# Kernel optimization log

Measured on AMD Instinct MI355X. Metric: run time of the kernel, lower is better.

## Reference

```python
import jax, jax.numpy as jnp
import numpy as np

INPUT_DIM = 768
HIDDEN = 64
NUM_CLASSES = 1


def _uniform(key, shape, bound):
    return jax.random.uniform(key, shape, jnp.float32, -bound, bound)


def setup_inputs() -> dict:
    key = jax.random.key(0)
    ks = jax.random.split(key, 16)
    B, T = 128, 512
    bound = 1.0 / np.sqrt(HIDDEN)  # PyTorch RNN init range
    inp = {
        "x": jax.random.normal(ks[0], (B, T, INPUT_DIM), jnp.float32),
        "fixation_num": 1,
        # layer 0: input_dim -> hidden
        "W_ih0": _uniform(ks[1], (HIDDEN, INPUT_DIM), bound),
        "W_hh0": _uniform(ks[2], (HIDDEN, HIDDEN), bound),
        "b_ih0": _uniform(ks[3], (HIDDEN,), bound),
        "b_hh0": _uniform(ks[4], (HIDDEN,), bound),
        # layer 1
        "W_ih1": _uniform(ks[5], (HIDDEN, HIDDEN), bound),
        "W_hh1": _uniform(ks[6], (HIDDEN, HIDDEN), bound),
        "b_ih1": _uniform(ks[7], (HIDDEN,), bound),
        "b_hh1": _uniform(ks[8], (HIDDEN,), bound),
        # layer 2
        "W_ih2": _uniform(ks[9], (HIDDEN, HIDDEN), bound),
        "W_hh2": _uniform(ks[10], (HIDDEN, HIDDEN), bound),
        "b_ih2": _uniform(ks[11], (HIDDEN,), bound),
        "b_hh2": _uniform(ks[12], (HIDDEN,), bound),
        # final linear head
        "fc_w": _uniform(ks[13], (NUM_CLASSES, HIDDEN), bound),
        "fc_b": _uniform(ks[14], (NUM_CLASSES,), bound),
    }
    return inp


def _rnn_layer(x, W_ih, W_hh, b_ih, b_hh):
    # x: [B, T, In] -> hidden sequence [B, T, H]; vanilla tanh RNN, h0 = 0
    pre = jnp.einsum("bti,hi->bth", x, W_ih) + b_ih + b_hh  # input projection for all t
    B = x.shape[0]
    h0 = jnp.zeros((B, W_hh.shape[0]), x.dtype)

    def step(h, p_t):  # p_t: [B, H]
        h = jnp.tanh(p_t + h @ W_hh.T)
        return h, h

    _, hs = jax.lax.scan(step, h0, jnp.swapaxes(pre, 0, 1))  # hs: [T, B, H]
    return jnp.swapaxes(hs, 0, 1)


def reference(x, fixation_num, W_ih0, W_hh0, b_ih0, b_hh0,
              W_ih1, W_hh1, b_ih1, b_hh1,
              W_ih2, W_hh2, b_ih2, b_hh2, fc_w, fc_b):
    # fixation_num is unused by the original forward
    h = _rnn_layer(x, W_ih0, W_hh0, b_ih0, b_hh0)
    h = _rnn_layer(h, W_ih1, W_hh1, b_ih1, b_hh1)
    h = _rnn_layer(h, W_ih2, W_hh2, b_ih2, b_hh2)
    last = h[:, -1, :]  # [B, H]
    return last @ fc_w.T + fc_b  # [B, num_classes]
```

## Files before the change

### kernel.cpp

```cpp
#include <hip/hip_runtime.h>


typedef __fp16 h2_t __attribute__((ext_vector_type(2)));
typedef __fp16 h8_t __attribute__((ext_vector_type(8)));
typedef float  f4_t __attribute__((ext_vector_type(4)));

union F4H  { float4 f; h2_t h[4]; };
union F4H8 { float4 f; h8_t h8; h2_t h2[4]; };
union H8U  { h2_t h2[4]; h8_t h8; };

__device__ __forceinline__ float fdot2(h2_t a, h2_t b, float c) {
    return __builtin_amdgcn_fdot2(a, b, c, false);
}
__device__ __forceinline__ h2_t pack_h2(float x, float y) {
    return __builtin_amdgcn_cvt_pkrtz(x, y);
}
__device__ __forceinline__ float tanh_fast(float x) {
    float e = __expf(2.0f * x);
    return 1.0f - 2.0f * __builtin_amdgcn_rcpf(e + 1.0f);
}

__global__ __launch_bounds__(256) void gemm_pre0(
    const float* __restrict__ x,
    const float* __restrict__ Wih,
    const float* __restrict__ bih, const float* __restrict__ bhh,
    float* __restrict__ pre0)
{
    const int tid = threadIdx.x;
    const int wv  = tid >> 6;
    const int l   = tid & 63;
    const int m   = l & 15;
    const int q   = l >> 4;
    const int rowB = blockIdx.x * 128 + wv * 32;

    const float* ax0 = x + (size_t)(rowB + m) * 768 + q * 8;
    const float* ax1 = x + (size_t)(rowB + 16 + m) * 768 + q * 8;

    float4 ar[2][2];
    float4 br[4][2];

    ar[0][0] = *(const float4*)ax0;       ar[0][1] = *(const float4*)(ax0 + 4);
    ar[1][0] = *(const float4*)ax1;       ar[1][1] = *(const float4*)(ax1 + 4);
#pragma unroll
    for (int nt = 0; nt < 4; ++nt) {
        const float* p = Wih + (size_t)(nt * 16 + m) * 768 + q * 8;
        br[nt][0] = *(const float4*)p;    br[nt][1] = *(const float4*)(p + 4);
    }

    f4_t acc[2][4];
#pragma unroll
    for (int mt = 0; mt < 2; ++mt)
#pragma unroll
        for (int nt = 0; nt < 4; ++nt)
#pragma unroll
            for (int i = 0; i < 4; ++i) acc[mt][nt][i] = 0.0f;

#pragma unroll
    for (int it = 0; it < 24; ++it) {
        H8U fa[2], fb[4];
#pragma unroll
        for (int mt = 0; mt < 2; ++mt) {
            fa[mt].h2[0] = pack_h2(ar[mt][0].x, ar[mt][0].y);
            fa[mt].h2[1] = pack_h2(ar[mt][0].z, ar[mt][0].w);
            fa[mt].h2[2] = pack_h2(ar[mt][1].x, ar[mt][1].y);
            fa[mt].h2[3] = pack_h2(ar[mt][1].z, ar[mt][1].w);
        }
#pragma unroll
        for (int nt = 0; nt < 4; ++nt) {
            fb[nt].h2[0] = pack_h2(br[nt][0].x, br[nt][0].y);
            fb[nt].h2[1] = pack_h2(br[nt][0].z, br[nt][0].w);
            fb[nt].h2[2] = pack_h2(br[nt][1].x, br[nt][1].y);
            fb[nt].h2[3] = pack_h2(br[nt][1].z, br[nt][1].w);
        }
        if (it + 1 < 24) {
            const int ko = (it + 1) * 32;
            ar[0][0] = *(const float4*)(ax0 + ko);
            ar[0][1] = *(const float4*)(ax0 + ko + 4);
            ar[1][0] = *(const float4*)(ax1 + ko);
            ar[1][1] = *(const float4*)(ax1 + ko + 4);
#pragma unroll
            for (int nt = 0; nt < 4; ++nt) {
                const float* p = Wih + (size_t)(nt * 16 + m) * 768 + q * 8 + ko;
                br[nt][0] = *(const float4*)p;
                br[nt][1] = *(const float4*)(p + 4);
            }
        }
#pragma unroll
        for (int mt = 0; mt < 2; ++mt)
#pragma unroll
            for (int nt = 0; nt < 4; ++nt)
                acc[mt][nt] = __builtin_amdgcn_mfma_f32_16x16x32_f16(
                    fa[mt].h8, fb[nt].h8, acc[mt][nt], 0, 0, 0);
    }

    float bn[4];
#pragma unroll
    for (int nt = 0; nt < 4; ++nt) bn[nt] = bih[nt * 16 + m] + bhh[nt * 16 + m];
#pragma unroll
    for (int mt = 0; mt < 2; ++mt)
#pragma unroll
        for (int i = 0; i < 4; ++i) {
            int row = rowB + mt * 16 + q * 4 + i;
            float* pr = pre0 + (size_t)row * 64 + m;
#pragma unroll
            for (int nt = 0; nt < 4; ++nt)
                pr[nt * 16] = acc[mt][nt][i] + bn[nt];
        }
}

__device__ __forceinline__ float layer_epoch(
    const __fp16* __restrict__ in0,
    __fp16* __restrict__ self0, int par,
    const h2_t* wB2, const h8_t* wX, float* __restrict__ xb,
    float bias, int j)
{
    __fp16*       selfPar  = self0 + par * 512;
    const __fp16* selfPrev = self0 + (par ^ 1) * 512;
    const int mm = j & 15;
    const int q4 = j >> 4;

    F4H8 A0, A1;
    const __fp16* arow = in0 + mm * 64 + q4 * 8;
    A0.f = *(const float4*)arow;
    A1.f = *(const float4*)(arow + 32);

    f4_t xacc[4];
#pragma unroll
    for (int nt = 0; nt < 4; ++nt) {
#pragma unroll
        for (int i = 0; i < 4; ++i) xacc[nt][i] = 0.0f;
        xacc[nt] = __builtin_amdgcn_mfma_f32_16x16x32_f16(
            A0.h8, wX[nt * 2 + 0], xacc[nt], 0, 0, 0);
        xacc[nt] = __builtin_amdgcn_mfma_f32_16x16x32_f16(
            A1.h8, wX[nt * 2 + 1], xacc[nt], 0, 0, 0);
    }
    if (j < 32) {
#pragma unroll
        for (int nt = 0; nt < 4; ++nt)
#pragma unroll
            for (int i = 0; i < 4; ++i)
                xb[(q4 * 4 + i) * 64 + nt * 16 + mm] = xacc[nt][i];
    }

    float hN = 0.0f;
#pragma unroll
    for (int s = 0; s < 8; ++s) {
        const __fp16* rc = (s == 0) ? (selfPrev + 7 * 64) : (selfPar + (s - 1) * 64);
        F4H uh[8];
#pragma unroll
        for (int qq = 0; qq < 8; ++qq) uh[qq].f = *(const float4*)(rc + qq * 8);
        float xs = xb[s * 64 + j];

        float a0 = 0.f, a1 = 0.f, a2 = 0.f, a3 = 0.f;
#pragma unroll
        for (int qq = 0; qq < 8; ++qq) {
            a0 = fdot2(wB2[qq * 4 + 0], uh[qq].h[0], a0);
            a1 = fdot2(wB2[qq * 4 + 1], uh[qq].h[1], a1);
            a2 = fdot2(wB2[qq * 4 + 2], uh[qq].h[2], a2);
            a3 = fdot2(wB2[qq * 4 + 3], uh[qq].h[3], a3);
        }
        hN = tanh_fast((a0 + a1) + (a2 + a3) + xs + bias);
        selfPar[s * 64 + j] = (__fp16)hN;
    }
    return hN;
}

__global__ __launch_bounds__(192, 1) void rnn_fused(
    const float* __restrict__ pre0,
    const float* __restrict__ Whh0,
    const float* __restrict__ Wih1, const float* __restrict__ Whh1,
    const float* __restrict__ bih1, const float* __restrict__ bhh1,
    const float* __restrict__ Wih2, const float* __restrict__ Whh2,
    const float* __restrict__ bih2, const float* __restrict__ bhh2,
    const float* __restrict__ fcw, const float* __restrict__ fcb,
    float* __restrict__ out)
{
    const int tid = threadIdx.x;
    const int g   = tid >> 6;
    const int j   = tid & 63;
    const int b   = blockIdx.x;

    __shared__ __align__(16) __fp16 hb[3][2][8][64];
    __shared__ __align__(16) float  xb2[2][8][64];

    const float* WB = (g == 0) ? Whh0 : ((g == 1) ? Whh1 : Whh2);
    h2_t wB2[32];
#pragma unroll
    for (int i = 0; i < 32; ++i)
        wB2[i] = pack_h2(WB[j * 64 + 2 * i], WB[j * 64 + 2 * i + 1]);

    const float* WX = (g == 1) ? Wih1 : ((g == 2) ? Wih2 : Whh0);
    const int mm = j & 15, q4 = j >> 4;
    h8_t wX[8];
#pragma unroll
    for (int nt = 0; nt < 4; ++nt)
#pragma unroll
        for (int c = 0; c < 2; ++c) {
            const float* p = WX + (nt * 16 + mm) * 64 + c * 32 + q4 * 8;
            float4 r0 = *(const float4*)p;
            float4 r1 = *(const float4*)(p + 4);
            H8U u;
            u.h2[0] = pack_h2(r0.x, r0.y); u.h2[1] = pack_h2(r0.z, r0.w);
            u.h2[2] = pack_h2(r1.x, r1.y); u.h2[3] = pack_h2(r1.z, r1.w);
            wX[nt * 2 + c] = u.h8;
        }

    const float bias = (g == 0) ? 0.0f
                     : ((g == 1) ? (bih1[j] + bhh1[j]) : (bih2[j] + bhh2[j]));

#pragma unroll
    for (int i = 0; i < 8; ++i) ((unsigned int*)hb)[tid + 192 * i] = 0u;

    const size_t pbase = (size_t)b * 32768;
    float pc[8], pn[8];
    if (g == 0) {
#pragma unroll
        for (int s = 0; s < 8; ++s) pc[s] = pre0[pbase + s * 64 + j];
    }
    __syncthreads();

    float hLast = 0.0f;

    for (int e = 0; e < 66; ++e) {
        if (g == 0) {
            if (e < 64) {
                if (e < 63) {
#pragma unroll
                    for (int s = 0; s < 8; ++s)
                        pn[s] = pre0[pbase + (size_t)(e + 1) * 512 + s * 64 + j];
                }
                const int par = e & 1;
#pragma unroll
                for (int s = 0; s < 8; ++s) {
                    const __fp16* rc = (s == 0) ? hb[0][par ^ 1][7] : hb[0][par][s - 1];
                    float a0 = 0.f, a1 = 0.f, a2 = 0.f, a3 = 0.f;
#pragma unroll
                    for (int qq = 0; qq < 8; ++qq) {
                        F4H u; u.f = *(const float4*)&rc[qq * 8];
                        a0 = fdot2(wB2[qq * 4 + 0], u.h[0], a0);
                        a1 = fdot2(wB2[qq * 4 + 1], u.h[1], a1);
                        a2 = fdot2(wB2[qq * 4 + 2], u.h[2], a2);
                        a3 = fdot2(wB2[qq * 4 + 3], u.h[3], a3);
                    }
                    float hN = tanh_fast((a0 + a1) + (a2 + a3) + pc[s]);
                    hb[0][par][s][j] = (__fp16)hN;
                }
#pragma unroll
                for (int s = 0; s < 8; ++s) pc[s] = pn[s];
            }
        } else if (g == 1) {
            if (e >= 1 && e < 65) {
                const int par = (e - 1) & 1;
                layer_epoch(&hb[0][par][0][0], &hb[1][0][0][0], par,
                            wB2, wX, &xb2[0][0][0], bias, j);
            }
        } else {
            if (e >= 2) {
                const int par = e & 1;
                float hN = layer_epoch(&hb[1][par][0][0], &hb[2][0][0][0], par,
                                       wB2, wX, &xb2[1][0][0], bias, j);
                if (e == 65) hLast = hN;
            }
        }
        __syncthreads();
    }

    if (g == 2) {
        float v = hLast * fcw[j];
#pragma unroll
        for (int m = 1; m < 64; m <<= 1) v += __shfl_xor(v, m, 64);
        if (j == 0) out[b] = v + fcb[0];
    }
}

extern "C" void kernel_launch(void* const* d_in, const int* in_sizes, int n_in,
                              void* d_out, int out_size, void* d_ws, size_t ws_size,
                              hipStream_t stream) {
    const float* x    = (const float*)d_in[0];
    const float* Wih0 = (const float*)d_in[2];
    const float* Whh0 = (const float*)d_in[3];
    const float* bih0 = (const float*)d_in[4];
    const float* bhh0 = (const float*)d_in[5];
    const float* Wih1 = (const float*)d_in[6];
    const float* Whh1 = (const float*)d_in[7];
    const float* bih1 = (const float*)d_in[8];
    const float* bhh1 = (const float*)d_in[9];
    const float* Wih2 = (const float*)d_in[10];
    const float* Whh2 = (const float*)d_in[11];
    const float* bih2 = (const float*)d_in[12];
    const float* bhh2 = (const float*)d_in[13];
    const float* fcw  = (const float*)d_in[14];
    const float* fcb  = (const float*)d_in[15];
    float* out  = (float*)d_out;
    float* pre0 = (float*)d_ws;

    gemm_pre0<<<512, 256, 0, stream>>>(x, Wih0, bih0, bhh0, pre0);
    rnn_fused<<<128, 192, 0, stream>>>(pre0, Whh0, Wih1, Whh1, bih1, bhh1,
                                       Wih2, Whh2, bih2, bhh2, fcw, fcb, out);
}
```

Before: 430.5 us.

## Prepack W_ih0 to fp16 fragments, shrink GEMM tile, widen RNN epochs to 16 steps

Adds a small kernel that converts W_ih0 once into fp16 MFMA fragments in workspace, so the input-projection GEMM loads packed B fragments instead of converting fp32 weights in every block. The GEMM uses 16 rows per wave with a two-deep register prefetch, doubling the grid. The fused 3-layer RNN pipeline now runs 16 timesteps per epoch instead of 8, halving the number of epochs and block-wide barriers, and the layer bias is folded into the MFMA projection output. Costs are more registers and LDS per block, plus an extra kernel launch.

```diff
diff --git a/kernel.cpp b/kernel.cpp
--- a/kernel.cpp
+++ b/kernel.cpp
@@ -20,9 +20,26 @@
     return 1.0f - 2.0f * __builtin_amdgcn_rcpf(e + 1.0f);
 }
 
+__global__ __launch_bounds__(256) void pack_wih(
+    const float* __restrict__ W, h8_t* __restrict__ wp)
+{
+    const int id = blockIdx.x * 256 + threadIdx.x;
+    if (id >= 24 * 4 * 64) return;
+    const int l  = id & 63;
+    const int nt = (id >> 6) & 3;
+    const int c  = id >> 8;
+    const float* p = W + (size_t)(nt * 16 + (l & 15)) * 768 + c * 32 + (l >> 4) * 8;
+    float4 r0 = *(const float4*)p;
+    float4 r1 = *(const float4*)(p + 4);
+    H8U u;
+    u.h2[0] = pack_h2(r0.x, r0.y); u.h2[1] = pack_h2(r0.z, r0.w);
+    u.h2[2] = pack_h2(r1.x, r1.y); u.h2[3] = pack_h2(r1.z, r1.w);
+    wp[id] = u.h8;
+}
+
 __global__ __launch_bounds__(256) void gemm_pre0(
     const float* __restrict__ x,
-    const float* __restrict__ Wih,
+    const h8_t* __restrict__ wp,
     const float* __restrict__ bih, const float* __restrict__ bhh,
     float* __restrict__ pre0)
 {
@@ -31,91 +48,74 @@
     const int l   = tid & 63;
     const int m   = l & 15;
     const int q   = l >> 4;
-    const int rowB = blockIdx.x * 128 + wv * 32;
-
-    const float* ax0 = x + (size_t)(rowB + m) * 768 + q * 8;
-    const float* ax1 = x + (size_t)(rowB + 16 + m) * 768 + q * 8;
+    const int rowB = blockIdx.x * 64 + wv * 16;
+
+    const float* ax = x + (size_t)(rowB + m) * 768 + q * 8;
 
     float4 ar[2][2];
-    float4 br[4][2];
-
-    ar[0][0] = *(const float4*)ax0;       ar[0][1] = *(const float4*)(ax0 + 4);
-    ar[1][0] = *(const float4*)ax1;       ar[1][1] = *(const float4*)(ax1 + 4);
-#pragma unroll
-    for (int nt = 0; nt < 4; ++nt) {
-        const float* p = Wih + (size_t)(nt * 16 + m) * 768 + q * 8;
-        br[nt][0] = *(const float4*)p;    br[nt][1] = *(const float4*)(p + 4);
-    }
-
-    f4_t acc[2][4];
-#pragma unroll
-    for (int mt = 0; mt < 2; ++mt)
+    h8_t   bf[2][4];
+
+#pragma unroll
+    for (int c = 0; c < 2; ++c) {
+        ar[c][0] = *(const float4*)(ax + c * 32);
+        ar[c][1] = *(const float4*)(ax + c * 32 + 4);
+        const int cb = c * 256 + l;
+        bf[c][0] = wp[cb];        bf[c][1] = wp[cb + 64];
+        bf[c][2] = wp[cb + 128];  bf[c][3] = wp[cb + 192];
+    }
+
+    f4_t acc[4];
+#pragma unroll
+    for (int nt = 0; nt < 4; ++nt)
+#pragma unroll
+        for (int i = 0; i < 4; ++i) acc[nt][i] = 0.0f;
+
+#pragma unroll
+    for (int it = 0; it < 24; ++it) {
+        const int bs = it & 1;
+        H8U fa;
+        fa.h2[0] = pack_h2(ar[bs][0].x, ar[bs][0].y);
+        fa.h2[1] = pack_h2(ar[bs][0].z, ar[bs][0].w);
+        fa.h2[2] = pack_h2(ar[bs][1].x, ar[bs][1].y);
+        fa.h2[3] = pack_h2(ar[bs][1].z, ar[bs][1].w);
+        h8_t fb0 = bf[bs][0], fb1 = bf[bs][1], fb2 = bf[bs][2], fb3 = bf[bs][3];
+
+        if (it + 2 < 24) {
+            const int ko = (it + 2) * 32;
+            ar[bs][0] = *(const float4*)(ax + ko);
+            ar[bs][1] = *(const float4*)(ax + ko + 4);
+            const int cb = (it + 2) * 256 + l;
+            bf[bs][0] = wp[cb];        bf[bs][1] = wp[cb + 64];
+            bf[bs][2] = wp[cb + 128];  bf[bs][3] = wp[cb + 192];
+        }
+
+        acc[0] = __builtin_amdgcn_mfma_f32_16x16x32_f16(fa.h8, fb0, acc[0], 0, 0, 0);
+        acc[1] = __builtin_amdgcn_mfma_f32_16x16x32_f16(fa.h8, fb1, acc[1], 0, 0, 0);
+        acc[2] = __builtin_amdgcn_mfma_f32_16x16x32_f16(fa.h8, fb2, acc[2], 0, 0, 0);
+        acc[3] = __builtin_amdgcn_mfma_f32_16x16x32_f16(fa.h8, fb3, acc[3], 0, 0, 0);
+    }
+
+    float bn[4];
+#pragma unroll
+    for (int nt = 0; nt < 4; ++nt) bn[nt] = bih[nt * 16 + m] + bhh[nt * 16 + m];
+#pragma unroll
+    for (int i = 0; i < 4; ++i) {
+        int row = rowB + q * 4 + i;
+        float* pr = pre0 + (size_t)row * 64 + m;
 #pragma unroll
         for (int nt = 0; nt < 4; ++nt)
-#pragma unroll
-            for (int i = 0; i < 4; ++i) acc[mt][nt][i] = 0.0f;
-
-#pragma unroll
-    for (int it = 0; it < 24; ++it) {
-        H8U fa[2], fb[4];
-#pragma unroll
-        for (int mt = 0; mt < 2; ++mt) {
-            fa[mt].h2[0] = pack_h2(ar[mt][0].x, ar[mt][0].y);
-            fa[mt].h2[1] = pack_h2(ar[mt][0].z, ar[mt][0].w);
-            fa[mt].h2[2] = pack_h2(ar[mt][1].x, ar[mt][1].y);
-            fa[mt].h2[3] = pack_h2(ar[mt][1].z, ar[mt][1].w);
-        }
-#pragma unroll
-        for (int nt = 0; nt < 4; ++nt) {
-            fb[nt].h2[0] = pack_h2(br[nt][0].x, br[nt][0].y);
-            fb[nt].h2[1] = pack_h2(br[nt][0].z, br[nt][0].w);
-            fb[nt].h2[2] = pack_h2(br[nt][1].x, br[nt][1].y);
-            fb[nt].h2[3] = pack_h2(br[nt][1].z, br[nt][1].w);
-        }
-        if (it + 1 < 24) {
-            const int ko = (it + 1) * 32;
-            ar[0][0] = *(const float4*)(ax0 + ko);
-            ar[0][1] = *(const float4*)(ax0 + ko + 4);
-            ar[1][0] = *(const float4*)(ax1 + ko);
-            ar[1][1] = *(const float4*)(ax1 + ko + 4);
-#pragma unroll
-            for (int nt = 0; nt < 4; ++nt) {
-                const float* p = Wih + (size_t)(nt * 16 + m) * 768 + q * 8 + ko;
-                br[nt][0] = *(const float4*)p;
-                br[nt][1] = *(const float4*)(p + 4);
-            }
-        }
-#pragma unroll
-        for (int mt = 0; mt < 2; ++mt)
-#pragma unroll
-            for (int nt = 0; nt < 4; ++nt)
-                acc[mt][nt] = __builtin_amdgcn_mfma_f32_16x16x32_f16(
-                    fa[mt].h8, fb[nt].h8, acc[mt][nt], 0, 0, 0);
-    }
-
-    float bn[4];
-#pragma unroll
-    for (int nt = 0; nt < 4; ++nt) bn[nt] = bih[nt * 16 + m] + bhh[nt * 16 + m];
-#pragma unroll
-    for (int mt = 0; mt < 2; ++mt)
-#pragma unroll
-        for (int i = 0; i < 4; ++i) {
-            int row = rowB + mt * 16 + q * 4 + i;
-            float* pr = pre0 + (size_t)row * 64 + m;
-#pragma unroll
-            for (int nt = 0; nt < 4; ++nt)
-                pr[nt * 16] = acc[mt][nt][i] + bn[nt];
-        }
+            pr[nt * 16] = acc[nt][i] + bn[nt];
+    }
 }
 
 __device__ __forceinline__ float layer_epoch(
     const __fp16* __restrict__ in0,
     __fp16* __restrict__ self0, int par,
     const h2_t* wB2, const h8_t* wX, float* __restrict__ xb,
-    float bias, int j)
+    const float* bias4, int j)
 {
-    __fp16*       selfPar  = self0 + par * 512;
-    const __fp16* selfPrev = self0 + (par ^ 1) * 512;
+    __fp16*       selfPar  = self0 + par * 1024;
+    const __fp16* selfPrev = self0 + (par ^ 1) * 1024;
     const int mm = j & 15;
     const int q4 = j >> 4;
 
@@ -134,22 +134,23 @@
         xacc[nt] = __builtin_amdgcn_mfma_f32_16x16x32_f16(
             A1.h8, wX[nt * 2 + 1], xacc[nt], 0, 0, 0);
     }
-    if (j < 32) {
-#pragma unroll
-        for (int nt = 0; nt < 4; ++nt)
-#pragma unroll
-            for (int i = 0; i < 4; ++i)
-                xb[(q4 * 4 + i) * 64 + nt * 16 + mm] = xacc[nt][i];
-    }
+#pragma unroll
+    for (int nt = 0; nt < 4; ++nt)
+#pragma unroll
+        for (int i = 0; i < 4; ++i)
+            xb[(q4 * 4 + i) * 64 + nt * 16 + mm] = xacc[nt][i] + bias4[nt];
+
+    float xs[16];
+#pragma unroll
+    for (int s = 0; s < 16; ++s) xs[s] = xb[s * 64 + j];
 
     float hN = 0.0f;
 #pragma unroll
-    for (int s = 0; s < 8; ++s) {
-        const __fp16* rc = (s == 0) ? (selfPrev + 7 * 64) : (selfPar + (s - 1) * 64);
+    for (int s = 0; s < 16; ++s) {
+        const __fp16* rc = (s == 0) ? (selfPrev + 15 * 64) : (selfPar + (s - 1) * 64);
         F4H uh[8];
 #pragma unroll
         for (int qq = 0; qq < 8; ++qq) uh[qq].f = *(const float4*)(rc + qq * 8);
-        float xs = xb[s * 64 + j];
 
         float a0 = 0.f, a1 = 0.f, a2 = 0.f, a3 = 0.f;
 #pragma unroll
@@ -159,7 +160,7 @@
             a2 = fdot2(wB2[qq * 4 + 2], uh[qq].h[2], a2);
             a3 = fdot2(wB2[qq * 4 + 3], uh[qq].h[3], a3);
         }
-        hN = tanh_fast((a0 + a1) + (a2 + a3) + xs + bias);
+        hN = tanh_fast((a0 + a1) + (a2 + a3) + xs[s]);
         selfPar[s * 64 + j] = (__fp16)hN;
     }
     return hN;
@@ -180,8 +181,8 @@
     const int j   = tid & 63;
     const int b   = blockIdx.x;
 
-    __shared__ __align__(16) __fp16 hb[3][2][8][64];
-    __shared__ __align__(16) float  xb2[2][8][64];
+    __shared__ __align__(16) __fp16 hb[3][2][16][64];
+    __shared__ __align__(16) float  xb2[2][16][64];
 
     const float* WB = (g == 0) ? Whh0 : ((g == 1) ? Whh1 : Whh2);
     h2_t wB2[32];
@@ -205,34 +206,39 @@
             wX[nt * 2 + c] = u.h8;
         }
 
-    const float bias = (g == 0) ? 0.0f
-                     : ((g == 1) ? (bih1[j] + bhh1[j]) : (bih2[j] + bhh2[j]));
-
-#pragma unroll
-    for (int i = 0; i < 8; ++i) ((unsigned int*)hb)[tid + 192 * i] = 0u;
+    float bias4[4];
+#pragma unroll
+    for (int nt = 0; nt < 4; ++nt) {
+        const int col = nt * 16 + mm;
+        bias4[nt] = (g == 1) ? (bih1[col] + bhh1[col])
+                  : ((g == 2) ? (bih2[col] + bhh2[col]) : 0.0f);
+    }
+
+#pragma unroll
+    for (int i = 0; i < 16; ++i) ((unsigned int*)hb)[tid + 192 * i] = 0u;
 
     const size_t pbase = (size_t)b * 32768;
-    float pc[8], pn[8];
+    float pc[16], pn[16];
     if (g == 0) {
 #pragma unroll
-        for (int s = 0; s < 8; ++s) pc[s] = pre0[pbase + s * 64 + j];
+        for (int s = 0; s < 16; ++s) pc[s] = pre0[pbase + s * 64 + j];
     }
     __syncthreads();
 
     float hLast = 0.0f;
 
-    for (int e = 0; e < 66; ++e) {
+    for (int e = 0; e < 34; ++e) {
         if (g == 0) {
-            if (e < 64) {
-                if (e < 63) {
-#pragma unroll
-                    for (int s = 0; s < 8; ++s)
-                        pn[s] = pre0[pbase + (size_t)(e + 1) * 512 + s * 64 + j];
+            if (e < 32) {
+                if (e < 31) {
+#pragma unroll
+                    for (int s = 0; s < 16; ++s)
+                        pn[s] = pre0[pbase + (size_t)(e + 1) * 1024 + s * 64 + j];
                 }
                 const int par = e & 1;
 #pragma unroll
-                for (int s = 0; s < 8; ++s) {
-                    const __fp16* rc = (s == 0) ? hb[0][par ^ 1][7] : hb[0][par][s - 1];
+                for (int s = 0; s < 16; ++s) {
+                    const __fp16* rc = (s == 0) ? hb[0][par ^ 1][15] : hb[0][par][s - 1];
                     float a0 = 0.f, a1 = 0.f, a2 = 0.f, a3 = 0.f;
 #pragma unroll
                     for (int qq = 0; qq < 8; ++qq) {
@@ -246,20 +252,20 @@
                     hb[0][par][s][j] = (__fp16)hN;
                 }
 #pragma unroll
-                for (int s = 0; s < 8; ++s) pc[s] = pn[s];
+                for (int s = 0; s < 16; ++s) pc[s] = pn[s];
             }
         } else if (g == 1) {
-            if (e >= 1 && e < 65) {
+            if (e >= 1 && e < 33) {
                 const int par = (e - 1) & 1;
                 layer_epoch(&hb[0][par][0][0], &hb[1][0][0][0], par,
-                            wB2, wX, &xb2[0][0][0], bias, j);
+                            wB2, wX, &xb2[0][0][0], bias4, j);
             }
         } else {
             if (e >= 2) {
                 const int par = e & 1;
                 float hN = layer_epoch(&hb[1][par][0][0], &hb[2][0][0][0], par,
-                                       wB2, wX, &xb2[1][0][0], bias, j);
-                if (e == 65) hLast = hN;
+                                       wB2, wX, &xb2[1][0][0], bias4, j);
+                if (e == 33) hLast = hN;
             }
         }
         __syncthreads();
@@ -293,8 +299,10 @@
     const float* fcb  = (const float*)d_in[15];
     float* out  = (float*)d_out;
     float* pre0 = (float*)d_ws;
-
-    gemm_pre0<<<512, 256, 0, stream>>>(x, Wih0, bih0, bhh0, pre0);
+    h8_t* wpack = (h8_t*)((char*)d_ws + (size_t)65536 * 64 * 4);
+
+    pack_wih<<<24, 256, 0, stream>>>(Wih0, wpack);
+    gemm_pre0<<<1024, 256, 0, stream>>>(x, wpack, bih0, bhh0, pre0);
     rnn_fused<<<128, 192, 0, stream>>>(pre0, Whh0, Wih1, Whh1, bih1, bhh1,
                                        Wih2, Whh2, bih2, bhh2, fcw, fcb, out);
 }
```

After: 414.4 us. 3.7% less time.
